# Performance work log

Hardware: AMD Instinct MI355X
Metric: run time of the kernel (lower is better)

## Reference

```python
import jax, jax.numpy as jnp
import numpy as np

MAX_SEQ_LEN = 1024
EMBED_DIM = 64


def setup_inputs() -> dict:
    key = jax.random.key(0)
    k1, k2, k3 = jax.random.split(key, 3)
    B, H, L, D = 2, 16, 1024, EMBED_DIM
    q = jax.random.normal(k1, (B, H, L, D), dtype=jnp.float32)
    k = jax.random.normal(k2, (B, H, L, D), dtype=jnp.float32)
    pos_emb = jax.random.normal(k3, (2 * MAX_SEQ_LEN - 1, D), dtype=jnp.float32)
    return {"q": q, "k": k, "pos_emb": pos_emb}


def reference(q, k, pos_emb):
    q_len = q.shape[2]
    k_len = k.shape[2]
    # relative distance index matrix, shifted and clamped into table range
    idx = jnp.arange(q_len)[:, None] - jnp.arange(k_len)[None, :] + (MAX_SEQ_LEN - 1)
    idx = jnp.clip(idx, 0, 2 * MAX_SEQ_LEN - 2)
    rel_emb = pos_emb[idx]  # [q_len, k_len, D]  (the O(Q*K*D) gather)
    # per-query batched contraction over head dim D
    bias = jnp.einsum('bhqd,qkd->bhqk', q, rel_emb)
    return bias / jnp.sqrt(jnp.asarray(EMBED_DIM, dtype=q.dtype))
```

## Files before the change

kernel.cpp:

```cpp
#include <hip/hip_runtime.h>
#include <hip/hip_bf16.h>
#include <stdint.h>


#define LSEQ 1024
#define DDIM 64

typedef __attribute__((ext_vector_type(8))) short bf16x8;
typedef __attribute__((ext_vector_type(16))) float f32x16;

__device__ __forceinline__ unsigned short f2b(float f) {
  union { float f; unsigned u; } c; c.f = f;
  unsigned u = c.u;
  u += 0x7fffu + ((u >> 16) & 1u);
  return (unsigned short)(u >> 16);
}

__global__ __launch_bounds__(256) void cvt_kernel(
    const float4* __restrict__ q4, const float4* __restrict__ p4,
    ushort4* __restrict__ qb, ushort4* __restrict__ pb) {
  int i = blockIdx.x * 256 + threadIdx.x;
  if (i < 524288) {
    float4 v = q4[i];
    ushort4 o;
    o.x = f2b(v.x * 0.125f); o.y = f2b(v.y * 0.125f);
    o.z = f2b(v.z * 0.125f); o.w = f2b(v.w * 0.125f);
    qb[i] = o;
  } else {
    int j = i - 524288;
    if (j < 32752) {
      float4 v = p4[j];
      ushort4 o;
      o.x = f2b(v.x); o.y = f2b(v.y); o.z = f2b(v.z); o.w = f2b(v.w);
      pb[j] = o;
    }
  }
}

__global__ __launch_bounds__(256) void rpe_kernel(
    const short* __restrict__ Qb, const short* __restrict__ Pb,
    float* __restrict__ out) {
  const int q    = blockIdx.x;
  const int lane = threadIdx.x & 63;
  const int wave = threadIdx.x >> 6;
  const int l31  = lane & 31;
  const int hi   = lane >> 5;

  bf16x8 a[4];
  const short* qp = Qb + (l31 * LSEQ + q) * DDIM + hi * 8;
#pragma unroll
  for (int s = 0; s < 4; ++s)
    a[s] = *(const bf16x8*)(qp + 16 * s);

  const int nbase = wave * 256;
#pragma unroll
  for (int t = 0; t < 8; ++t) {
    const int n0 = nbase + 32 * t;
    const short* pp = Pb + (q + 1023 - n0 - l31) * DDIM + hi * 8;
    f32x16 acc;
#pragma unroll
    for (int r = 0; r < 16; ++r) acc[r] = 0.0f;
#pragma unroll
    for (int s = 0; s < 4; ++s) {
      bf16x8 b = *(const bf16x8*)(pp + 16 * s);
      acc = __builtin_amdgcn_mfma_f32_32x32x16_bf16(a[s], b, acc, 0, 0, 0);
    }
    float* obase = out + (size_t)hi * 4 * LSEQ * LSEQ + q * LSEQ + n0 + l31;
#pragma unroll
    for (int r = 0; r < 16; ++r) {
      int m = (r & 3) + 8 * (r >> 2);
      obase[(size_t)m * (LSEQ * LSEQ)] = acc[r];
    }
  }
}

extern "C" void kernel_launch(void* const* d_in, const int* in_sizes, int n_in,
                              void* d_out, int out_size, void* d_ws, size_t ws_size,
                              hipStream_t stream) {
  const float* qin = (const float*)d_in[0];
  const float* pin = (const float*)d_in[2];

  short* qb = (short*)d_ws;
  short* pb = (short*)d_ws + 2097152;

  cvt_kernel<<<2176, 256, 0, stream>>>((const float4*)qin, (const float4*)pin,
                                       (ushort4*)qb, (ushort4*)pb);
  rpe_kernel<<<1024, 256, 0, stream>>>(qb, pb, (float*)d_out);
}
```

Before: 40.39 us.

## Stage pos_emb tiles through double-buffered swizzled LDS via async global_load_lds

Each wave now prefetches its next 32-row pos_emb tile into a per-wave double-buffered LDS region with global_load_lds, using an XOR swizzle to avoid bank conflicts. MFMA B fragments are read from LDS instead of directly from global memory, with manual vmcnt waits overlapping loads of tile t+1 with compute and stores of tile t. The goal is to hide global load latency for the B operand. The hand-tuned vmcnt counts must match the actual number of outstanding memory ops, including the output stores, and the last iteration issues a wasted wraparound prefetch.

```diff
diff --git a/kernel.cpp b/kernel.cpp
--- a/kernel.cpp
+++ b/kernel.cpp
@@ -40,36 +40,69 @@
 __global__ __launch_bounds__(256) void rpe_kernel(
     const short* __restrict__ Qb, const short* __restrict__ Pb,
     float* __restrict__ out) {
+  __shared__ short lds[4][2][2048];
   const int q    = blockIdx.x;
-  const int lane = threadIdx.x & 63;
-  const int wave = threadIdx.x >> 6;
+  const int tid  = (int)threadIdx.x;
+  const int lane = tid & 63;
+  const int wave = tid >> 6;
   const int l31  = lane & 31;
   const int hi   = lane >> 5;
+  const int nbase = wave << 8;
+
+  const int lane_off = ((lane >> 3) << 7) + ((((lane & 7) ^ (lane >> 3))) << 4);
+  const char* Pc = (const char*)Pb;
+
+  {
+    const int lo = q + 992 - nbase;
+    const char* src = Pc + ((size_t)lo << 7) + lane_off;
+#pragma unroll
+    for (int j = 0; j < 4; ++j)
+      __builtin_amdgcn_global_load_lds(
+          (const __attribute__((address_space(1))) void*)(src + (j << 10)),
+          (__attribute__((address_space(3))) void*)&lds[wave][0][j << 9],
+          16, 0, 0);
+  }
 
   bf16x8 a[4];
-  const short* qp = Qb + (l31 * LSEQ + q) * DDIM + hi * 8;
+  const short* qp = Qb + ((l31 << 10) + q) * DDIM + (hi << 3);
 #pragma unroll
   for (int s = 0; s < 4; ++s)
     a[s] = *(const bf16x8*)(qp + 16 * s);
 
-  const int nbase = wave * 256;
+  const int rr = 31 - l31;
+  const int rx = rr & 7;
+
 #pragma unroll
   for (int t = 0; t < 8; ++t) {
-    const int n0 = nbase + 32 * t;
-    const short* pp = Pb + (q + 1023 - n0 - l31) * DDIM + hi * 8;
+    {
+      const int tn = (t + 1) & 7;
+      const int b  = (t + 1) & 1;
+      const int lo = q + 992 - nbase - (tn << 5);
+      const char* src = Pc + ((size_t)lo << 7) + lane_off;
+#pragma unroll
+      for (int j = 0; j < 4; ++j)
+        __builtin_amdgcn_global_load_lds(
+            (const __attribute__((address_space(1))) void*)(src + (j << 10)),
+            (__attribute__((address_space(3))) void*)&lds[wave][b][j << 9],
+            16, 0, 0);
+    }
+    if (t == 0) asm volatile("s_waitcnt vmcnt(4)" ::: "memory");
+    else        asm volatile("s_waitcnt vmcnt(20)" ::: "memory");
+
+    const short* base = &lds[wave][t & 1][rr << 6];
     f32x16 acc;
 #pragma unroll
     for (int r = 0; r < 16; ++r) acc[r] = 0.0f;
 #pragma unroll
     for (int s = 0; s < 4; ++s) {
-      bf16x8 b = *(const bf16x8*)(pp + 16 * s);
-      acc = __builtin_amdgcn_mfma_f32_32x32x16_bf16(a[s], b, acc, 0, 0, 0);
+      bf16x8 bfr = *(const bf16x8*)(base + (((hi + 2 * s) ^ rx) << 3));
+      acc = __builtin_amdgcn_mfma_f32_32x32x16_bf16(a[s], bfr, acc, 0, 0, 0);
     }
-    float* obase = out + (size_t)hi * 4 * LSEQ * LSEQ + q * LSEQ + n0 + l31;
+    float* obase = out + ((size_t)hi << 22) + (q << 10) + nbase + (t << 5) + l31;
 #pragma unroll
     for (int r = 0; r < 16; ++r) {
-      int m = (r & 3) + 8 * (r >> 2);
-      obase[(size_t)m * (LSEQ * LSEQ)] = acc[r];
+      const int m = (r & 3) + 8 * (r >> 2);
+      obase[(size_t)m << 20] = acc[r];
     }
   }
 }
```

After: 38.44 us. 1.05x faster.
